# Kernel tuning notes

Measured on AMD Instinct MI355X. Metric: run time of the kernel, lower is better.

The kernel has to match this reference:

```python
import jax, jax.numpy as jnp
import numpy as np

# ---- static hash-grid config (instant-NGP style, matches tcnn hash.json) ----
N_LEVELS = 16
F_PER_LEVEL = 2
LOG2_T = 19
TABLE_SIZE = 2 ** LOG2_T          # 524288 entries per level
BASE_RES = 16
PER_LEVEL_SCALE = 1.3819          # finest res ~2048
RES = [int(np.floor(BASE_RES * PER_LEVEL_SCALE ** l)) for l in range(N_LEVELS)]
N_POINTS = 2 ** 21
PRIME_Y = np.uint32(2654435761)   # tcnn spatial-hash prime

_CORNERS = jnp.array([[0, 0], [1, 0], [0, 1], [1, 1]], dtype=jnp.uint32)


def _level_features(x, table, res):
    """Bilinear hash-grid lookup for one level. x: [N,2] in [0,1). -> [N,F]."""
    pos = x * res                      # [N,2]
    x0f = jnp.floor(pos)
    w = pos - x0f                      # interpolation fractions [N,2]
    x0 = x0f.astype(jnp.uint32)
    c = x0[:, None, :] + _CORNERS[None]            # [N,4,2] corner coords
    if (res + 1) ** 2 <= TABLE_SIZE:
        # dense grid fits in the table: linear indexing (as tcnn does)
        idx = c[..., 0] + c[..., 1] * jnp.uint32(res + 1)
    else:
        # spatial hash with uint32 wraparound
        idx = (c[..., 0] ^ (c[..., 1] * PRIME_Y)) & jnp.uint32(TABLE_SIZE - 1)
    feats = table[idx.astype(jnp.int32)]           # [N,4,F] irregular gather
    wx = jnp.where(_CORNERS[None, :, 0] == 1, w[:, None, 0], 1.0 - w[:, None, 0])
    wy = jnp.where(_CORNERS[None, :, 1] == 1, w[:, None, 1], 1.0 - w[:, None, 1])
    return jnp.sum(feats * (wx * wy)[..., None], axis=1)  # [N,F]


def setup_inputs() -> dict:
    key = jax.random.key(0)
    k1, k2, k3, k4, k5 = jax.random.split(key, 5)
    x = jax.random.uniform(k1, (N_POINTS, 2), dtype=jnp.float32)
    # tcnn hash tables are initialized uniform in [-1e-4, 1e-4]
    tables = jax.random.uniform(k2, (N_LEVELS, TABLE_SIZE, F_PER_LEVEL),
                                dtype=jnp.float32, minval=-1e-4, maxval=1e-4)
    d_in = 2 + N_LEVELS * F_PER_LEVEL  # 34
    h = 64
    w1 = jax.random.normal(k3, (d_in, h), dtype=jnp.float32) * (1.0 / np.sqrt(d_in))
    w2 = jax.random.normal(k4, (h, h), dtype=jnp.float32) * (1.0 / np.sqrt(h))
    w3 = jax.random.normal(k5, (h, 3), dtype=jnp.float32) * (1.0 / np.sqrt(h))
    return {"x": x, "tables": tables, "w1": w1, "w2": w2, "w3": w3}


def reference(x, tables, w1, w2, w3):
    # multi-res hash grid encode (16 levels, static small loop)
    feats = [_level_features(x, tables[l], RES[l]) for l in range(N_LEVELS)]
    enc = jnp.concatenate([x] + feats, axis=1)     # [N, 2 + 32]
    # tiny fused MLP decode (no biases, as in tcnn networks)
    h = jax.nn.relu(enc @ w1)
    h = jax.nn.relu(h @ w2)
    return h @ w3                                   # [N, 3]
```

## Files before the change

kernel.cpp:

```cpp
#include <hip/hip_runtime.h>

typedef unsigned int u32;
typedef unsigned short u16;
typedef __attribute__((ext_vector_type(8))) short s16x8;
typedef __attribute__((ext_vector_type(4))) float f32x4;
typedef float f32x4a __attribute__((ext_vector_type(4), aligned(8)));
typedef u32  u32x2a  __attribute__((ext_vector_type(2), aligned(4)));

#define TBL    524288u
#define TMASK  (TBL - 1u)
#define HPRIME 2654435761u
#define NBINS  16384
#define NBLK   256

__device__ constexpr int RESI[16] = {16,22,30,42,58,80,111,153,212,294,406,561,775,1072,1481,2047};

static __device__ __forceinline__ u16 f2bf(float f){
  u32 u = __builtin_bit_cast(u32, f);
  return (u16)((u + 0x7fffu + ((u >> 16) & 1u)) >> 16);
}
static __device__ __forceinline__ float bf2f(u16 h){ return __builtin_bit_cast(float, (u32)h << 16); }
static __device__ __forceinline__ float blo(u32 e){ return __builtin_bit_cast(float, (u32)(e << 16)); }
static __device__ __forceinline__ float bhi(u32 e){ return __builtin_bit_cast(float, (u32)(e & 0xffff0000u)); }
static __device__ __forceinline__ u32 packbf2(float a, float b){ return (u32)f2bf(a) | ((u32)f2bf(b) << 16); }
static __device__ __forceinline__ u32 cvtpk(float a, float b){
  u32 r; asm("v_cvt_pk_bf16_f32 %0, %1, %2" : "=v"(r) : "v"(a), "v"(b)); return r;
}
static __device__ __forceinline__ u32 spread8(u32 v){
  v &= 0xFFu;
  v = (v | (v << 4)) & 0x0F0Fu;
  v = (v | (v << 2)) & 0x3333u;
  v = (v | (v << 1)) & 0x5555u;
  return v;
}
static __device__ __forceinline__ u32 mkey(float x, float y){
  u32 kx = (u32)(x * 128.f); kx = kx > 127u ? 127u : kx;
  u32 ky = (u32)(y * 128.f); ky = ky > 127u ? 127u : ky;
  return spread8(kx) | (spread8(ky) << 1);
}

#define MFMA(A,B,C) __builtin_amdgcn_mfma_f32_16x16x32_bf16((A),(B),(C),0,0,0)

__global__ __launch_bounds__(256) void cvt_tab(const float4* __restrict__ src,
                                               uint2* __restrict__ dst, int n4) {
  for (int i = blockIdx.x*256 + threadIdx.x; i < n4; i += gridDim.x*256) {
    const float4 v = src[i];
    dst[i] = make_uint2(packbf2(v.x, v.y), packbf2(v.z, v.w));
  }
}

__global__ __launch_bounds__(256) void histb_k(const float2* __restrict__ xq,
                                               u32* __restrict__ bh, int ppb) {
  __shared__ u32 cnt[NBINS];
  const int j = blockIdx.x;
  for (int i = threadIdx.x; i < NBINS; i += 256) cnt[i] = 0;
  __syncthreads();
  const float2* p = xq + (size_t)j * ppb;
  for (int i = threadIdx.x; i < ppb; i += 256) {
    const float2 v = p[i];
    atomicAdd(&cnt[mkey(v.x, v.y)], 1u);
  }
  __syncthreads();
  u32* o = bh + (size_t)j * NBINS;
  for (int i = threadIdx.x; i < NBINS; i += 256) o[i] = cnt[i];
}
__global__ __launch_bounds__(256) void scanb_k(u32* __restrict__ bh, u32* __restrict__ tot) {
  const int b = blockIdx.x*256 + threadIdx.x;
  u32 run = 0;
  for (int j = 0; j < NBLK; ++j) {
    const size_t k = (size_t)j * NBINS + b;
    const u32 v = bh[k]; bh[k] = run; run += v;
  }
  tot[b] = run;
}
__global__ __launch_bounds__(1024) void scant_k(u32* __restrict__ tot) {
  __shared__ u32 part[1024];
  const int t = threadIdx.x;
  u32 loc[16]; u32 s = 0;
  #pragma unroll
  for (int i = 0; i < 16; ++i) { loc[i] = tot[t*16 + i]; s += loc[i]; }
  part[t] = s;
  __syncthreads();
  for (int d = 1; d < 1024; d <<= 1) {
    const u32 v = (t >= d) ? part[t - d] : 0u;
    __syncthreads();
    part[t] += v;
    __syncthreads();
  }
  u32 run = part[t] - s;
  #pragma unroll
  for (int i = 0; i < 16; ++i) { tot[t*16 + i] = run; run += loc[i]; }
}
__global__ __launch_bounds__(256) void scatb_k(const float2* __restrict__ xq,
                                               const u32* __restrict__ bh,
                                               const u32* __restrict__ binst,
                                               float2* __restrict__ xs,
                                               u32* __restrict__ perm, int ppb) {
  __shared__ u32 offs[NBINS];
  const int j = blockIdx.x;
  for (int i = threadIdx.x; i < NBINS; i += 256)
    offs[i] = bh[(size_t)j * NBINS + i] + binst[i];
  __syncthreads();
  const size_t base = (size_t)j * ppb;
  for (int i = threadIdx.x; i < ppb; i += 256) {
    const float2 pt = xq[base + i];
    const u32 pos = atomicAdd(&offs[mkey(pt.x, pt.y)], 1u);
    xs[pos] = pt;
    perm[pos] = (u32)(base + i);
  }
}

template<bool PACKED, bool SORT>
__global__ __launch_bounds__(256, 2) void ngp_fused(
    const float2* __restrict__ xq,
    const float2* __restrict__ tab32,
    const u32*    __restrict__ ctab,
    const u32*    __restrict__ perm,
    const float*  __restrict__ w1,
    const float*  __restrict__ w2,
    const float*  __restrict__ w3,
    float* __restrict__ out,
    int iters)
{
  __shared__ __align__(16) u16   encS[256 * 40];
  __shared__ __align__(16) float xyS [256 * 2];
  __shared__ __align__(16) u16   hS  [4][2][16*72];
  __shared__ __align__(16) s16x8 wS  [10][64];

  const int tid  = threadIdx.x;
  const int lane = tid & 63;
  const int wv   = tid >> 6;
  const int m    = lane & 15;
  const int q    = lane >> 4;

  float w1x[4], w1y[4];
  s16x8 B1[4], B2h[4][2], B3h[2];
  #pragma unroll
  for (int c = 0; c < 4; ++c) {
    const int n = c*16 + m;
    w1x[c] = w1[n]; w1y[c] = w1[64 + n];
    s16x8 f1;
    #pragma unroll
    for (int j = 0; j < 8; ++j) {
      const int k = q*8 + j;
      f1[j] = (short)f2bf(w1[(2 + k)*64 + n]);
    }
    B1[c] = f1;
    #pragma unroll
    for (int s = 0; s < 2; ++s) {
      s16x8 fh, fl;
      #pragma unroll
      for (int j = 0; j < 8; ++j) {
        const int k = s*32 + q*8 + j;
        const float v = w2[k*64 + n];
        const u16 h = f2bf(v);
        fh[j] = (short)h; fl[j] = (short)f2bf(v - bf2f(h));
      }
      B2h[c][s] = fh;
      if (wv == 0) wS[c*2 + s][lane] = fl;
    }
  }
  #pragma unroll
  for (int s = 0; s < 2; ++s) {
    s16x8 fh, fl;
    #pragma unroll
    for (int j = 0; j < 8; ++j) {
      const int k = s*32 + q*8 + j;
      const float v = (m < 3) ? w3[k*3 + m] : 0.f;
      const u16 h = f2bf(v);
      fh[j] = (short)h; fl[j] = (short)f2bf(v - bf2f(h));
    }
    B3h[s] = fh;
    if (wv == 0) wS[8 + s][lane] = fl;
  }
  __syncthreads();

  u16* const hpl = &hS[wv][0][0];
  u16* const lpl = &hS[wv][1][0];

  for (int it = 0; it < iters; ++it) {
    const int base = (blockIdx.x * iters + it) << 8;

    {
      const float2 xy = xq[base + tid];
      ((float2*)xyS)[tid] = xy;
      const float xf = xy.x, yf = xy.y;
      u32 er[16];
      u32 hv[4][4];
      float2 hv32[4][4];
      #pragma unroll
      for (int l = 12; l < 16; ++l) {
        const int res = RESI[l];
        const u32 ix = (u32)floorf(xf * (float)res);
        const u32 iy = (u32)floorf(yf * (float)res);
        const u32 hy = iy * HPRIME, hy1 = hy + HPRIME;
        const u32 i0 = ( ix       ^ hy ) & TMASK;
        const u32 i1 = ((ix + 1u) ^ hy ) & TMASK;
        const u32 i2 = ( ix       ^ hy1) & TMASK;
        const u32 i3 = ((ix + 1u) ^ hy1) & TMASK;
        if constexpr (PACKED) {
          const u32* t = ctab + (size_t)(l - 8) * TBL;
          hv[l-12][0] = t[i0]; hv[l-12][1] = t[i1];
          hv[l-12][2] = t[i2]; hv[l-12][3] = t[i3];
        } else {
          const float2* t = tab32 + (size_t)l * TBL;
          hv32[l-12][0] = t[i0]; hv32[l-12][1] = t[i1];
          hv32[l-12][2] = t[i2]; hv32[l-12][3] = t[i3];
        }
      }
      #pragma unroll
      for (int l = 0; l < 12; ++l) {
        const int res = RESI[l];
        const float px = xf * (float)res, py = yf * (float)res;
        const float fx = floorf(px), fy = floorf(py);
        const float wx = px - fx, wy = py - fy;
        const u32 ix = (u32)fx, iy = (u32)fy;
        const float w00 = (1.f-wx)*(1.f-wy), w10 = wx*(1.f-wy);
        const float w01 = (1.f-wx)*wy,       w11 = wx*wy;
        const u32 st  = (u32)res + 1u;
        const u32 i00 = ix + iy*st;
        float f0, f1;
        if (!PACKED || l < 8) {
          const float2* t = tab32 + (size_t)l * TBL;
          const f32x4a eA = *(const f32x4a*)&t[i00];
          const f32x4a eB = *(const f32x4a*)&t[i00 + st];
          f0 = eA[0]*w00 + eA[2]*w10 + eB[0]*w01 + eB[2]*w11;
          f1 = eA[1]*w00 + eA[3]*w10 + eB[1]*w01 + eB[3]*w11;
        } else {
          const u32* t = ctab + (size_t)(l - 8) * TBL;
          const u32x2a eA = *(const u32x2a*)&t[i00];
          const u32x2a eB = *(const u32x2a*)&t[i00 + st];
          f0 = blo(eA[0])*w00 + blo(eA[1])*w10 + blo(eB[0])*w01 + blo(eB[1])*w11;
          f1 = bhi(eA[0])*w00 + bhi(eA[1])*w10 + bhi(eB[0])*w01 + bhi(eB[1])*w11;
        }
        er[l] = cvtpk(f0, f1);
      }
      #pragma unroll
      for (int hl = 0; hl < 4; ++hl) {
        const int res = RESI[12 + hl];
        const float px = xf * (float)res, py = yf * (float)res;
        const float wx = px - floorf(px), wy = py - floorf(py);
        const float w00 = (1.f-wx)*(1.f-wy), w10 = wx*(1.f-wy);
        const float w01 = (1.f-wx)*wy,       w11 = wx*wy;
        float f0, f1;
        if constexpr (PACKED) {
          f0 = blo(hv[hl][0])*w00 + blo(hv[hl][1])*w10
             + blo(hv[hl][2])*w01 + blo(hv[hl][3])*w11;
          f1 = bhi(hv[hl][0])*w00 + bhi(hv[hl][1])*w10
             + bhi(hv[hl][2])*w01 + bhi(hv[hl][3])*w11;
        } else {
          f0 = hv32[hl][0].x*w00 + hv32[hl][1].x*w10 + hv32[hl][2].x*w01 + hv32[hl][3].x*w11;
          f1 = hv32[hl][0].y*w00 + hv32[hl][1].y*w10 + hv32[hl][2].y*w01 + hv32[hl][3].y*w11;
        }
        er[12 + hl] = cvtpk(f0, f1);
      }
      uint4* rowp = (uint4*)&encS[tid * 40];
      rowp[0] = make_uint4(er[0],  er[1],  er[2],  er[3]);
      rowp[1] = make_uint4(er[4],  er[5],  er[6],  er[7]);
      rowp[2] = make_uint4(er[8],  er[9],  er[10], er[11]);
      rowp[3] = make_uint4(er[12], er[13], er[14], er[15]);
    }

    #pragma unroll 1
    for (int t4 = 0; t4 < 4; ++t4) {
      const int rbase = wv*64 + t4*16;
      const s16x8 a1 = *(const s16x8*)&encS[(rbase + m)*40 + q*8];

      float xr[4], yr[4];
      #pragma unroll
      for (int r = 0; r < 4; ++r) {
        const float2 v = ((const float2*)xyS)[rbase + q*4 + r];
        xr[r] = v.x; yr[r] = v.y;
      }

      f32x4 acc[4];
      #pragma unroll
      for (int c = 0; c < 4; ++c) {
        f32x4 z;
        #pragma unroll
        for (int r = 0; r < 4; ++r) z[r] = xr[r]*w1x[c] + yr[r]*w1y[c];
        acc[c] = MFMA(a1, B1[c], z);
      }

      #pragma unroll
      for (int c = 0; c < 4; ++c)
        #pragma unroll
        for (int r = 0; r < 4; ++r) {
          const float h = fmaxf(acc[c][r], 0.f);
          const u32 hp_ = cvtpk(h, h);
          const float lf = h - __builtin_bit_cast(float, hp_ << 16);
          const u32 lp_ = cvtpk(lf, lf);
          const int idx = (q*4 + r)*72 + c*16 + m;
          hpl[idx] = (u16)hp_;
          lpl[idx] = (u16)lp_;
        }

      s16x8 hi0 = *(const s16x8*)&hpl[m*72 + q*8];
      s16x8 hi1 = *(const s16x8*)&hpl[m*72 + 32 + q*8];
      s16x8 lo0 = *(const s16x8*)&lpl[m*72 + q*8];
      s16x8 lo1 = *(const s16x8*)&lpl[m*72 + 32 + q*8];

      #pragma unroll
      for (int c = 0; c < 4; ++c) {
        const s16x8 b2l0 = wS[c*2 + 0][lane];
        const s16x8 b2l1 = wS[c*2 + 1][lane];
        f32x4 z = {0.f,0.f,0.f,0.f};
        z = MFMA(hi0, B2h[c][0], z); z = MFMA(hi1, B2h[c][1], z);
        z = MFMA(lo0, B2h[c][0], z); z = MFMA(lo1, B2h[c][1], z);
        z = MFMA(hi0, b2l0,      z); z = MFMA(hi1, b2l1,      z);
        acc[c] = z;
      }

      #pragma unroll
      for (int c = 0; c < 4; ++c)
        #pragma unroll
        for (int r = 0; r < 4; ++r) {
          const float h = fmaxf(acc[c][r], 0.f);
          const u32 hp_ = cvtpk(h, h);
          const float lf = h - __builtin_bit_cast(float, hp_ << 16);
          const u32 lp_ = cvtpk(lf, lf);
          const int idx = (q*4 + r)*72 + c*16 + m;
          hpl[idx] = (u16)hp_;
          lpl[idx] = (u16)lp_;
        }

      hi0 = *(const s16x8*)&hpl[m*72 + q*8];
      hi1 = *(const s16x8*)&hpl[m*72 + 32 + q*8];
      lo0 = *(const s16x8*)&lpl[m*72 + q*8];
      lo1 = *(const s16x8*)&lpl[m*72 + 32 + q*8];

      const s16x8 b3l0 = wS[8][lane];
      const s16x8 b3l1 = wS[9][lane];
      f32x4 z = {0.f,0.f,0.f,0.f};
      z = MFMA(hi0, B3h[0], z); z = MFMA(hi1, B3h[1], z);
      z = MFMA(lo0, B3h[0], z); z = MFMA(lo1, B3h[1], z);
      z = MFMA(hi0, b3l0,   z); z = MFMA(hi1, b3l1,   z);

      if (m < 3) {
        #pragma unroll
        for (int r = 0; r < 4; ++r) {
          const int pi = base + rbase + q*4 + r;
          const size_t oi = SORT ? (size_t)perm[pi] : (size_t)pi;
          out[oi*3 + m] = z[r];
        }
      }
    }
  }
}

extern "C" void kernel_launch(void* const* d_in, const int* in_sizes, int n_in,
                              void* d_out, int out_size, void* d_ws, size_t ws_size,
                              hipStream_t stream) {
  const int N = in_sizes[0] / 2;
  const int ITERS = 4;
  const int blocks = N / (256 * ITERS);
  const size_t ctab_b   = (size_t)8 * TBL * 4;
  const size_t xs_off   = ctab_b;
  const size_t perm_off = xs_off + (size_t)N * 8;
  const size_t bh_off   = perm_off + (size_t)N * 4;
  const size_t tot_off  = bh_off + (size_t)NBLK * NBINS * 4;
  const size_t need     = tot_off + (size_t)NBINS * 4;

  char* ws = (char*)d_ws;
  if (ws_size >= need && (N % NBLK) == 0) {
    const int ppb = N / NBLK;
    cvt_tab<<<2048, 256, 0, stream>>>(((const float4*)d_in[1]) + (size_t)4*TBL,
                                      (uint2*)d_ws, (int)(4*TBL));
    u32* bh    = (u32*)(ws + bh_off);
    u32* tot   = (u32*)(ws + tot_off);
    float2* xs = (float2*)(ws + xs_off);
    u32* perm  = (u32*)(ws + perm_off);
    histb_k<<<NBLK, 256, 0, stream>>>((const float2*)d_in[0], bh, ppb);
    scanb_k<<<NBINS/256, 256, 0, stream>>>(bh, tot);
    scant_k<<<1, 1024, 0, stream>>>(tot);
    scatb_k<<<NBLK, 256, 0, stream>>>((const float2*)d_in[0], bh, tot, xs, perm, ppb);
    ngp_fused<true, true><<<blocks, 256, 0, stream>>>(
        xs, (const float2*)d_in[1], (const u32*)d_ws, perm,
        (const float*)d_in[2], (const float*)d_in[3], (const float*)d_in[4],
        (float*)d_out, ITERS);
  } else if (ws_size >= ctab_b) {
    cvt_tab<<<2048, 256, 0, stream>>>(((const float4*)d_in[1]) + (size_t)4*TBL,
                                      (uint2*)d_ws, (int)(4*TBL));
    ngp_fused<true, false><<<blocks, 256, 0, stream>>>(
        (const float2*)d_in[0], (const float2*)d_in[1], (const u32*)d_ws, nullptr,
        (const float*)d_in[2], (const float*)d_in[3], (const float*)d_in[4],
        (float*)d_out, ITERS);
  } else {
    ngp_fused<false, false><<<blocks, 256, 0, stream>>>(
        (const float2*)d_in[0], (const float2*)d_in[1], (const u32*)d_ws, nullptr,
        (const float*)d_in[2], (const float*)d_in[3], (const float*)d_in[4],
        (float*)d_out, ITERS);
  }
}
```

Baseline: 377.1 us.

## Parallelize block-histogram scan hierarchically, shrink histograms to u16, swizzle block order

The serial per-bin scan over 256 block histograms, which used only 64 blocks, is replaced by a three-stage hierarchical scan: group sums, a scan over 16 groups, then a per-group rescan. This exposes far more parallelism to cut sort-preprocessing latency. Histogram counts are stored as u16 to halve their traffic, which holds because each block handles 8192 points, though a single bin reaching 65536 would overflow. The fused kernel also remaps blockIdx so that concurrently running blocks take spatially separated chunks of the sorted points, adding two extra kernel launches overall.

```diff
diff --git a/kernel.cpp b/kernel.cpp
--- a/kernel.cpp
+++ b/kernel.cpp
@@ -12,6 +12,8 @@
 #define HPRIME 2654435761u
 #define NBINS  16384
 #define NBLK   256
+#define NGRP   16
+#define GSZ    16
 
 __device__ constexpr int RESI[16] = {16,22,30,42,58,80,111,153,212,294,406,561,775,1072,1481,2047};
 
@@ -50,7 +52,7 @@
 }
 
 __global__ __launch_bounds__(256) void histb_k(const float2* __restrict__ xq,
-                                               u32* __restrict__ bh, int ppb) {
+                                               u16* __restrict__ bh, int ppb) {
   __shared__ u32 cnt[NBINS];
   const int j = blockIdx.x;
   for (int i = threadIdx.x; i < NBINS; i += 256) cnt[i] = 0;
@@ -61,15 +63,25 @@
     atomicAdd(&cnt[mkey(v.x, v.y)], 1u);
   }
   __syncthreads();
-  u32* o = bh + (size_t)j * NBINS;
-  for (int i = threadIdx.x; i < NBINS; i += 256) o[i] = cnt[i];
-}
-__global__ __launch_bounds__(256) void scanb_k(u32* __restrict__ bh, u32* __restrict__ tot) {
+  u16* o = bh + (size_t)j * NBINS;
+  for (int i = threadIdx.x; i < NBINS; i += 256) o[i] = (u16)cnt[i];
+}
+__global__ __launch_bounds__(256) void scang1_k(const u16* __restrict__ bh,
+                                                u32* __restrict__ gs) {
+  const int t = blockIdx.x*256 + threadIdx.x;
+  const int g = t / NBINS, b = t % NBINS;
+  u32 s = 0;
+  #pragma unroll
+  for (int k = 0; k < GSZ; ++k) s += bh[(size_t)(g*GSZ + k)*NBINS + b];
+  gs[t] = s;
+}
+__global__ __launch_bounds__(256) void scang2_k(u32* __restrict__ gs, u32* __restrict__ tot) {
   const int b = blockIdx.x*256 + threadIdx.x;
   u32 run = 0;
-  for (int j = 0; j < NBLK; ++j) {
-    const size_t k = (size_t)j * NBINS + b;
-    const u32 v = bh[k]; bh[k] = run; run += v;
+  #pragma unroll
+  for (int g = 0; g < NGRP; ++g) {
+    const size_t k = (size_t)g*NBINS + b;
+    const u32 v = gs[k]; gs[k] = run; run += v;
   }
   tot[b] = run;
 }
@@ -91,15 +103,26 @@
   #pragma unroll
   for (int i = 0; i < 16; ++i) { tot[t*16 + i] = run; run += loc[i]; }
 }
+__global__ __launch_bounds__(256) void scang3_k(u16* __restrict__ bh,
+                                                const u32* __restrict__ gs) {
+  const int t = blockIdx.x*256 + threadIdx.x;
+  const int g = t / NBINS, b = t % NBINS;
+  u32 run = gs[t];
+  #pragma unroll
+  for (int k = 0; k < GSZ; ++k) {
+    const size_t idx = (size_t)(g*GSZ + k)*NBINS + b;
+    const u32 v = bh[idx]; bh[idx] = (u16)run; run += v;
+  }
+}
 __global__ __launch_bounds__(256) void scatb_k(const float2* __restrict__ xq,
-                                               const u32* __restrict__ bh,
+                                               const u16* __restrict__ bh,
                                                const u32* __restrict__ binst,
                                                float2* __restrict__ xs,
                                                u32* __restrict__ perm, int ppb) {
   __shared__ u32 offs[NBINS];
   const int j = blockIdx.x;
   for (int i = threadIdx.x; i < NBINS; i += 256)
-    offs[i] = bh[(size_t)j * NBINS + i] + binst[i];
+    offs[i] = (u32)bh[(size_t)j * NBINS + i] + binst[i];
   __syncthreads();
   const size_t base = (size_t)j * ppb;
   for (int i = threadIdx.x; i < ppb; i += 256) {
@@ -133,6 +156,8 @@
   const int m    = lane & 15;
   const int q    = lane >> 4;
 
+  const int wb = ((blockIdx.x & 7) * (int)(gridDim.x >> 3)) + (blockIdx.x >> 3);
+
   float w1x[4], w1y[4];
   s16x8 B1[4], B2h[4][2], B3h[2];
   #pragma unroll
@@ -179,7 +204,7 @@
   u16* const lpl = &hS[wv][1][0];
 
   for (int it = 0; it < iters; ++it) {
-    const int base = (blockIdx.x * iters + it) << 8;
+    const int base = (wb * iters + it) << 8;
 
     {
       const float2 xy = xq[base + tid];
@@ -358,21 +383,25 @@
   const size_t xs_off   = ctab_b;
   const size_t perm_off = xs_off + (size_t)N * 8;
   const size_t bh_off   = perm_off + (size_t)N * 4;
-  const size_t tot_off  = bh_off + (size_t)NBLK * NBINS * 4;
+  const size_t gs_off   = bh_off + (size_t)NBLK * NBINS * 2;
+  const size_t tot_off  = gs_off + (size_t)NGRP * NBINS * 4;
   const size_t need     = tot_off + (size_t)NBINS * 4;
 
   char* ws = (char*)d_ws;
-  if (ws_size >= need && (N % NBLK) == 0) {
+  if (ws_size >= need && (N % NBLK) == 0 && (blocks % 8) == 0) {
     const int ppb = N / NBLK;
     cvt_tab<<<2048, 256, 0, stream>>>(((const float4*)d_in[1]) + (size_t)4*TBL,
                                       (uint2*)d_ws, (int)(4*TBL));
-    u32* bh    = (u32*)(ws + bh_off);
+    u16* bh    = (u16*)(ws + bh_off);
+    u32* gs    = (u32*)(ws + gs_off);
     u32* tot   = (u32*)(ws + tot_off);
     float2* xs = (float2*)(ws + xs_off);
     u32* perm  = (u32*)(ws + perm_off);
     histb_k<<<NBLK, 256, 0, stream>>>((const float2*)d_in[0], bh, ppb);
-    scanb_k<<<NBINS/256, 256, 0, stream>>>(bh, tot);
+    scang1_k<<<NGRP*NBINS/256, 256, 0, stream>>>(bh, gs);
+    scang2_k<<<NBINS/256, 256, 0, stream>>>(gs, tot);
     scant_k<<<1, 1024, 0, stream>>>(tot);
+    scang3_k<<<NGRP*NBINS/256, 256, 0, stream>>>(bh, gs);
     scatb_k<<<NBLK, 256, 0, stream>>>((const float2*)d_in[0], bh, tot, xs, perm, ppb);
     ngp_fused<true, true><<<blocks, 256, 0, stream>>>(
         xs, (const float2*)d_in[1], (const u32*)d_ws, perm,
```

After: 371.8 us. No clear change (-1.4%).

## Fuse table conversion into histogram, collapse scan kernels, remap block order

Applied to the files above, without the earlier changes.

Folds the bf16 table conversion into the histogram kernel and halves the sort bins to 8192 by coarsening the y key. Per-block counts are stored as u16, and the two scan kernels are replaced by one per-bin block scan, with the bin-total prefix now recomputed inside the scatter kernel. This cuts kernel launches and the histogram traffic. The main kernel also remaps block indices in strides of eight, presumably to spread spatially sorted work across XCDs for cache locality. The trade-offs are a coarser sort key, which weakens gather locality, plus a redundant 8192-element scan in every scatter block and a binscan launch of 8192 blocks doing strided u16 reads.

```diff
diff --git a/kernel.cpp b/kernel.cpp
--- a/kernel.cpp
+++ b/kernel.cpp
@@ -10,7 +10,7 @@
 #define TBL    524288u
 #define TMASK  (TBL - 1u)
 #define HPRIME 2654435761u
-#define NBINS  16384
+#define NBINS  8192
 #define NBLK   256
 
 __device__ constexpr int RESI[16] = {16,22,30,42,58,80,111,153,212,294,406,561,775,1072,1481,2047};
@@ -35,7 +35,7 @@
 }
 static __device__ __forceinline__ u32 mkey(float x, float y){
   u32 kx = (u32)(x * 128.f); kx = kx > 127u ? 127u : kx;
-  u32 ky = (u32)(y * 128.f); ky = ky > 127u ? 127u : ky;
+  u32 ky = (u32)(y * 64.f);  ky = ky > 63u  ? 63u  : ky;
   return spread8(kx) | (spread8(ky) << 1);
 }
 
@@ -49,10 +49,16 @@
   }
 }
 
-__global__ __launch_bounds__(256) void histb_k(const float2* __restrict__ xq,
-                                               u32* __restrict__ bh, int ppb) {
+__global__ __launch_bounds__(256) void cvthist_k(const float4* __restrict__ src,
+                                                 uint2* __restrict__ dst, int n4,
+                                                 const float2* __restrict__ xq,
+                                                 u16* __restrict__ bh, int ppb) {
   __shared__ u32 cnt[NBINS];
   const int j = blockIdx.x;
+  for (int i = j*256 + threadIdx.x; i < n4; i += NBLK*256) {
+    const float4 v = src[i];
+    dst[i] = make_uint2(packbf2(v.x, v.y), packbf2(v.z, v.w));
+  }
   for (int i = threadIdx.x; i < NBINS; i += 256) cnt[i] = 0;
   __syncthreads();
   const float2* p = xq + (size_t)j * ppb;
@@ -61,48 +67,55 @@
     atomicAdd(&cnt[mkey(v.x, v.y)], 1u);
   }
   __syncthreads();
-  u32* o = bh + (size_t)j * NBINS;
-  for (int i = threadIdx.x; i < NBINS; i += 256) o[i] = cnt[i];
-}
-__global__ __launch_bounds__(256) void scanb_k(u32* __restrict__ bh, u32* __restrict__ tot) {
-  const int b = blockIdx.x*256 + threadIdx.x;
-  u32 run = 0;
-  for (int j = 0; j < NBLK; ++j) {
-    const size_t k = (size_t)j * NBINS + b;
-    const u32 v = bh[k]; bh[k] = run; run += v;
-  }
-  tot[b] = run;
-}
-__global__ __launch_bounds__(1024) void scant_k(u32* __restrict__ tot) {
-  __shared__ u32 part[1024];
-  const int t = threadIdx.x;
-  u32 loc[16]; u32 s = 0;
-  #pragma unroll
-  for (int i = 0; i < 16; ++i) { loc[i] = tot[t*16 + i]; s += loc[i]; }
-  part[t] = s;
-  __syncthreads();
-  for (int d = 1; d < 1024; d <<= 1) {
-    const u32 v = (t >= d) ? part[t - d] : 0u;
+  u16* o = bh + (size_t)j * NBINS;
+  for (int i = threadIdx.x; i < NBINS; i += 256) o[i] = (u16)cnt[i];
+}
+__global__ __launch_bounds__(256) void binscan_k(u16* __restrict__ bh, u32* __restrict__ tot) {
+  __shared__ u32 sc[256];
+  const int b = blockIdx.x;
+  const int k = threadIdx.x;
+  const size_t idx = (size_t)k * NBINS + b;
+  const u32 v = bh[idx];
+  sc[k] = v;
+  __syncthreads();
+  for (int d = 1; d < 256; d <<= 1) {
+    const u32 t = (k >= d) ? sc[k - d] : 0u;
     __syncthreads();
-    part[t] += v;
+    sc[k] += t;
     __syncthreads();
   }
-  u32 run = part[t] - s;
-  #pragma unroll
-  for (int i = 0; i < 16; ++i) { tot[t*16 + i] = run; run += loc[i]; }
+  bh[idx] = (u16)(sc[k] - v);
+  if (k == 255) tot[b] = sc[255];
 }
 __global__ __launch_bounds__(256) void scatb_k(const float2* __restrict__ xq,
-                                               const u32* __restrict__ bh,
-                                               const u32* __restrict__ binst,
+                                               const u16* __restrict__ bh,
+                                               const u32* __restrict__ tot,
                                                float2* __restrict__ xs,
                                                u32* __restrict__ perm, int ppb) {
   __shared__ u32 offs[NBINS];
+  __shared__ u32 red[256];
   const int j = blockIdx.x;
-  for (int i = threadIdx.x; i < NBINS; i += 256)
-    offs[i] = bh[(size_t)j * NBINS + i] + binst[i];
+  const int t = threadIdx.x;
+  u32 loc[32]; u32 s = 0;
+  #pragma unroll
+  for (int i = 0; i < 32; ++i) { loc[i] = tot[t*32 + i]; s += loc[i]; }
+  red[t] = s;
+  __syncthreads();
+  for (int d = 1; d < 256; d <<= 1) {
+    const u32 v = (t >= d) ? red[t - d] : 0u;
+    __syncthreads();
+    red[t] += v;
+    __syncthreads();
+  }
+  u32 run = red[t] - s;
+  #pragma unroll
+  for (int i = 0; i < 32; ++i) {
+    offs[t*32 + i] = run + (u32)bh[(size_t)j * NBINS + t*32 + i];
+    run += loc[i];
+  }
   __syncthreads();
   const size_t base = (size_t)j * ppb;
-  for (int i = threadIdx.x; i < ppb; i += 256) {
+  for (int i = t; i < ppb; i += 256) {
     const float2 pt = xq[base + i];
     const u32 pos = atomicAdd(&offs[mkey(pt.x, pt.y)], 1u);
     xs[pos] = pt;
@@ -133,6 +146,8 @@
   const int m    = lane & 15;
   const int q    = lane >> 4;
 
+  const int wb = ((blockIdx.x & 7) * (int)(gridDim.x >> 3)) + (blockIdx.x >> 3);
+
   float w1x[4], w1y[4];
   s16x8 B1[4], B2h[4][2], B3h[2];
   #pragma unroll
@@ -179,7 +194,7 @@
   u16* const lpl = &hS[wv][1][0];
 
   for (int it = 0; it < iters; ++it) {
-    const int base = (blockIdx.x * iters + it) << 8;
+    const int base = (wb * iters + it) << 8;
 
     {
       const float2 xy = xq[base + tid];
@@ -358,21 +373,20 @@
   const size_t xs_off   = ctab_b;
   const size_t perm_off = xs_off + (size_t)N * 8;
   const size_t bh_off   = perm_off + (size_t)N * 4;
-  const size_t tot_off  = bh_off + (size_t)NBLK * NBINS * 4;
+  const size_t tot_off  = bh_off + (size_t)NBLK * NBINS * 2;
   const size_t need     = tot_off + (size_t)NBINS * 4;
 
   char* ws = (char*)d_ws;
-  if (ws_size >= need && (N % NBLK) == 0) {
+  if (ws_size >= need && (N % NBLK) == 0 && (blocks % 8) == 0) {
     const int ppb = N / NBLK;
-    cvt_tab<<<2048, 256, 0, stream>>>(((const float4*)d_in[1]) + (size_t)4*TBL,
-                                      (uint2*)d_ws, (int)(4*TBL));
-    u32* bh    = (u32*)(ws + bh_off);
+    u16* bh    = (u16*)(ws + bh_off);
     u32* tot   = (u32*)(ws + tot_off);
     float2* xs = (float2*)(ws + xs_off);
     u32* perm  = (u32*)(ws + perm_off);
-    histb_k<<<NBLK, 256, 0, stream>>>((const float2*)d_in[0], bh, ppb);
-    scanb_k<<<NBINS/256, 256, 0, stream>>>(bh, tot);
-    scant_k<<<1, 1024, 0, stream>>>(tot);
+    cvthist_k<<<NBLK, 256, 0, stream>>>(((const float4*)d_in[1]) + (size_t)4*TBL,
+                                        (uint2*)d_ws, (int)(4*TBL),
+                                        (const float2*)d_in[0], bh, ppb);
+    binscan_k<<<NBINS, 256, 0, stream>>>(bh, tot);
     scatb_k<<<NBLK, 256, 0, stream>>>((const float2*)d_in[0], bh, tot, xs, perm, ppb);
     ngp_fused<true, true><<<blocks, 256, 0, stream>>>(
         xs, (const float2*)d_in[1], (const u32*)d_ws, perm,
```

After: 382.1 us. No clear change (+1.3%).
